# Optimization experiments

Measured on AMD Instinct MI355X. Metric: run time of the kernel, lower is better.

## Reference

```python
import jax, jax.numpy as jnp
import numpy as np

T_DATA, E_NO, I_NO, SUB_NO = 10000, 2000, 500, 64
KERN_LEN, PAD = 201, 100


def setup_inputs() -> dict:
    key = jax.random.key(0)
    ks = jax.random.split(key, 8)
    S_e = (jax.random.uniform(ks[0], (T_DATA, E_NO)) < 0.05).astype(jnp.float32)
    S_i = (jax.random.uniform(ks[1], (T_DATA, I_NO)) < 0.05).astype(jnp.float32)
    # Synapse->subunit assignment: each synapse feeds exactly one subunit (one-hot rows of C_syn.T)
    ae = jax.random.randint(ks[2], (E_NO,), 0, SUB_NO)
    ai = jax.random.randint(ks[3], (I_NO,), 0, SUB_NO)
    C_syn_e = jax.nn.one_hot(ae, SUB_NO, dtype=jnp.float32).T  # [sub_no, E_no]
    C_syn_i = jax.nn.one_hot(ai, SUB_NO, dtype=jnp.float32).T  # [sub_no, I_no]
    # Sparse dendritic coupling matrix (binary tree-like connectivity)
    C_den = (jax.random.uniform(ks[4], (SUB_NO, SUB_NO)) < 0.05).astype(jnp.float32)
    # Learned raw parameters (per __init__: ones * init)
    weight_raw = jnp.zeros((SUB_NO, 2), jnp.float32)          # weight_init = 0.0
    decay_raw = jnp.full((SUB_NO,), 2.0, jnp.float32)         # decay_init = 2.0
    threshold_raw = jnp.zeros((SUB_NO,), jnp.float32)         # threshold_init = 0.0
    prop_raw = jnp.full((SUB_NO,), -1.0, jnp.float32)         # prop_init = -1.0
    return {"S_e": S_e, "S_i": S_i, "C_den": C_den, "C_syn_e": C_syn_e,
            "C_syn_i": C_syn_i, "weight_raw": weight_raw, "decay_raw": decay_raw,
            "threshold_raw": threshold_raw, "prop_raw": prop_raw}


def reference(S_e, S_i, C_den, C_syn_e, C_syn_i, weight_raw, decay_raw, threshold_raw, prop_raw):
    sub_no = C_den.shape[0]
    # Project presynaptic spikes onto subunits: [T, sub_no]
    syn_e = S_e @ C_syn_e.T
    syn_i = S_i @ C_syn_i.T
    weight_e = jnp.exp(weight_raw[:, 0])
    weight_i = -jnp.exp(weight_raw[:, 1])
    decay = jax.nn.sigmoid(decay_raw)
    threshold = -jnp.exp(threshold_raw)
    prop = jnpp = jnp.exp(prop_raw)
    drive = syn_e * weight_e[None, :] + syn_i * weight_i[None, :]  # [T, sub_no]

    def step_fn(carry, d_t):
        V, spk = carry
        # reset-on-spike, leak, synaptic drive, dendritic propagation of spikes
        V = V * (1.0 - spk) * decay + d_t + (spk * prop) @ C_den.T
        spk = jnp.heaviside(V + threshold, jnp.float32(0.0))
        return (V, spk), spk

    init = (jnp.zeros(sub_no, jnp.float32), jnp.zeros(sub_no, jnp.float32))
    _, spk_out = jax.lax.scan(step_fn, init, drive)  # spk_out: [T, sub_no]

    # Alpha-kernel smoothing of root subunit spike train (Tau, W are fixed buffers)
    t_tau = jnp.arange(KERN_LEN, dtype=jnp.float32) / jnp.exp(jnp.float32(2.0))
    kern = t_tau * jnp.exp(-t_tau) * jnp.exp(jnp.float32(0.75))
    kern_flipped = jnp.flip(kern)
    x = spk_out[:, 0][None, None, :]               # [1,1,T]
    w = kern_flipped[None, None, :]                # [1,1,201]
    final = jax.lax.conv_general_dilated(x, w, (1,), [(PAD, PAD)]).reshape(-1)
    return final, spk_out
```

## Files before the change

### kernel.cpp

```cpp
#include <hip/hip_runtime.h>
#include <math.h>

#define T_DATA 10000
#define E_NO 2000
#define I_NO 500
#define SUB_NO 64
#define KERN_LEN 201
#define PAD 100
#define NBLK 314

__global__ void assign_kernel(const float* __restrict__ Ce, const float* __restrict__ Ci,
                              int* __restrict__ ae, int* __restrict__ ai) {
    int idx = blockIdx.x * 256 + threadIdx.x;
    if (idx < E_NO) {
        int a = 0;
        for (int s = 0; s < SUB_NO; ++s)
            if (Ce[(size_t)s * E_NO + idx] != 0.0f) a = s;
        ae[idx] = a;
    } else if (idx < E_NO + I_NO) {
        int i = idx - E_NO;
        int a = 0;
        for (int s = 0; s < SUB_NO; ++s)
            if (Ci[(size_t)s * I_NO + i] != 0.0f) a = s;
        ai[i] = a;
    }
}

__global__ void drive_kernel(const float* __restrict__ Se, const float* __restrict__ Si,
                             const float* __restrict__ wraw,
                             const int* __restrict__ ae, const int* __restrict__ ai,
                             float* __restrict__ drive) {
    __shared__ float be[SUB_NO];
    __shared__ float bi[SUB_NO];
    int t = blockIdx.x;
    int tid = threadIdx.x;
    if (tid < SUB_NO) { be[tid] = 0.0f; bi[tid] = 0.0f; }
    __syncthreads();
    const float4* se4 = (const float4*)(Se + (size_t)t * E_NO);
    for (int e4 = tid; e4 < E_NO / 4; e4 += 256) {
        float4 v = se4[e4];
        int b = e4 * 4;
        if (v.x != 0.0f) atomicAdd(&be[ae[b + 0]], 1.0f);
        if (v.y != 0.0f) atomicAdd(&be[ae[b + 1]], 1.0f);
        if (v.z != 0.0f) atomicAdd(&be[ae[b + 2]], 1.0f);
        if (v.w != 0.0f) atomicAdd(&be[ae[b + 3]], 1.0f);
    }
    const float4* si4 = (const float4*)(Si + (size_t)t * I_NO);
    for (int i4 = tid; i4 < I_NO / 4; i4 += 256) {
        float4 v = si4[i4];
        int b = i4 * 4;
        if (v.x != 0.0f) atomicAdd(&bi[ai[b + 0]], 1.0f);
        if (v.y != 0.0f) atomicAdd(&bi[ai[b + 1]], 1.0f);
        if (v.z != 0.0f) atomicAdd(&bi[ai[b + 2]], 1.0f);
        if (v.w != 0.0f) atomicAdd(&bi[ai[b + 3]], 1.0f);
    }
    __syncthreads();
    if (tid < SUB_NO) {
        float we = (float)exp((double)wraw[2 * tid]);
        float wi = -(float)exp((double)wraw[2 * tid + 1]);
        drive[(size_t)t * SUB_NO + tid] =
            __fadd_rn(__fmul_rn(be[tid], we), __fmul_rn(bi[tid], wi));
    }
}

#define S_LIN(DK, DK1, LIT) \
  "v_and_b32 %[tlo], vcc_lo, %[rlo]\n\t" \
  "v_and_b32 %[thi], vcc_hi, %[rhi]\n\t" \
  "v_cndmask_b32 %[base], %[w0], %[" DK "], vcc\n\t" \
  "v_bcnt_u32_b32 %[kc], %[tlo], 0\n\t" \
  "v_bcnt_u32_b32 %[kc], %[thi], %[kc]\n\t" \
  "v_cvt_f32_u32 %[kf], %[kc]\n\t" \
  "v_mul_f32 %[acc], %[kf], %[pp]\n\t" \
  "v_add_f32 %[vv], %[base], %[acc]\n\t" \
  "v_cmp_gt_f32 vcc, %[vv], %[thr]\n\t" \
  "v_mul_f32 %[w0], %[vv], %[dec]\n\t" \
  "v_add_f32 %[w0], %[w0], %[" DK1 "]\n\t" \
  "v_or_b32 %[tmp], " LIT ", %[bits]\n\t" \
  "v_cndmask_b32 %[bits], %[bits], %[tmp], vcc\n\t"

#define S_BP(DK, DK1, LIT) \
  "v_and_b32 %[tlo], vcc_lo, %[rlo]\n\t" \
  "v_and_b32 %[thi], vcc_hi, %[rhi]\n\t" \
  "v_cndmask_b32 %[base], %[w0], %[" DK "], vcc\n\t" \
  "v_bcnt_u32_b32 %[kc], %[tlo], 0\n\t" \
  "v_bcnt_u32_b32 %[kc], %[thi], %[kc]\n\t" \
  "v_lshlrev_b32 %[kc], 2, %[kc]\n\t" \
  "ds_bpermute_b32 %[acc], %[kc], %[vtab]\n\t" \
  "s_waitcnt lgkmcnt(0)\n\t" \
  "v_add_f32 %[vv], %[base], %[acc]\n\t" \
  "v_cmp_gt_f32 vcc, %[vv], %[thr]\n\t" \
  "v_mul_f32 %[w0], %[vv], %[dec]\n\t" \
  "v_add_f32 %[w0], %[w0], %[" DK1 "]\n\t" \
  "v_or_b32 %[tmp], " LIT ", %[bits]\n\t" \
  "v_cndmask_b32 %[bits], %[bits], %[tmp], vcc\n\t"

#define STEPS32(S) \
  S("d0","d1","1")            S("d1","d2","2")            S("d2","d3","4")            S("d3","d4","8") \
  S("d4","d5","16")           S("d5","d6","32")           S("d6","d7","64")           S("d7","d8","0x80") \
  S("d8","d9","0x100")        S("d9","d10","0x200")       S("d10","d11","0x400")      S("d11","d12","0x800") \
  S("d12","d13","0x1000")     S("d13","d14","0x2000")     S("d14","d15","0x4000")     S("d15","d16","0x8000") \
  S("d16","d17","0x10000")    S("d17","d18","0x20000")    S("d18","d19","0x40000")    S("d19","d20","0x80000") \
  S("d20","d21","0x100000")   S("d21","d22","0x200000")   S("d22","d23","0x400000")   S("d23","d24","0x800000") \
  S("d24","d25","0x1000000")  S("d25","d26","0x2000000")  S("d26","d27","0x4000000")  S("d27","d28","0x8000000") \
  S("d28","d29","0x10000000") S("d29","d30","0x20000000") S("d30","d31","0x40000000") S("d31","d32","0x80000000")

#define RUN_BLOCK(STEPSTR, B) do { \
    unsigned int _tlo, _thi, _kc, _tmp, _bits; float _kf, _acc, _base; \
    unsigned long long _mout; \
    asm volatile( \
        "s_mov_b64 vcc, %[min]\n\t" \
        "v_mov_b32 %[bits], 0\n\t" \
        "s_nop 1\n\t" \
        STEPSTR \
        "s_mov_b64 %[mout], vcc\n\t" \
        : [vv]"+v"(V), [w0]"+v"(w0), [bits]"=&v"(_bits), [mout]"=s"(_mout), \
          [tlo]"=&v"(_tlo), [thi]"=&v"(_thi), [kc]"=&v"(_kc), [tmp]"=&v"(_tmp), \
          [kf]"=&v"(_kf), [acc]"=&v"(_acc), [base]"=&v"(_base) \
        : [min]"s"(m), [rlo]"v"(row_lo), [rhi]"v"(row_hi), [pp]"v"(p0), \
          [dec]"v"(decay), [thr]"v"(thrpos), [vtab]"v"(vtab), \
          [d0]"v"(B[0]),  [d1]"v"(B[1]),  [d2]"v"(B[2]),  [d3]"v"(B[3]), \
          [d4]"v"(B[4]),  [d5]"v"(B[5]),  [d6]"v"(B[6]),  [d7]"v"(B[7]), \
          [d8]"v"(B[8]),  [d9]"v"(B[9]),  [d10]"v"(B[10]), [d11]"v"(B[11]), \
          [d12]"v"(B[12]), [d13]"v"(B[13]), [d14]"v"(B[14]), [d15]"v"(B[15]), \
          [d16]"v"(B[16]), [d17]"v"(B[17]), [d18]"v"(B[18]), [d19]"v"(B[19]), \
          [d20]"v"(B[20]), [d21]"v"(B[21]), [d22]"v"(B[22]), [d23]"v"(B[23]), \
          [d24]"v"(B[24]), [d25]"v"(B[25]), [d26]"v"(B[26]), [d27]"v"(B[27]), \
          [d28]"v"(B[28]), [d29]"v"(B[29]), [d30]"v"(B[30]), [d31]"v"(B[31]), \
          [d32]"v"(B[32]) \
        : "vcc"); \
    m = _mout; bitsv = _bits; } while (0)

__device__ void scan_lin_asm(const float* drive, unsigned int* packed,
                             unsigned int row_lo, unsigned int row_hi, float p0,
                             float decay, float thrpos, float vtab, int s) {
    const float* dp = drive + s;
    unsigned int* pw = packed + s;
    float bufA[33], bufB[33];
#pragma unroll
    for (int k = 0; k < 33; ++k) bufA[k] = dp[(size_t)k * SUB_NO];
    float V = 0.0f, w0 = bufA[0];
    unsigned long long m = 0ull;
    unsigned int bitsv;
    for (int b = 0; b < NBLK; b += 2) {
#pragma unroll
        for (int k = 0; k < 33; ++k) bufB[k] = dp[((size_t)(b + 1) * 32 + k) * SUB_NO];
        RUN_BLOCK(STEPS32(S_LIN), bufA);
        pw[(size_t)b * SUB_NO] = bitsv;
#pragma unroll
        for (int k = 0; k < 33; ++k) bufA[k] = dp[((size_t)(b + 2) * 32 + k) * SUB_NO];
        RUN_BLOCK(STEPS32(S_LIN), bufB);
        pw[(size_t)(b + 1) * SUB_NO] = bitsv;
    }
}

__device__ void scan_bp_asm(const float* drive, unsigned int* packed,
                            unsigned int row_lo, unsigned int row_hi, float p0,
                            float decay, float thrpos, float vtab, int s) {
    const float* dp = drive + s;
    unsigned int* pw = packed + s;
    float bufA[33], bufB[33];
#pragma unroll
    for (int k = 0; k < 33; ++k) bufA[k] = dp[(size_t)k * SUB_NO];
    float V = 0.0f, w0 = bufA[0];
    unsigned long long m = 0ull;
    unsigned int bitsv;
    for (int b = 0; b < NBLK; b += 2) {
#pragma unroll
        for (int k = 0; k < 33; ++k) bufB[k] = dp[((size_t)(b + 1) * 32 + k) * SUB_NO];
        RUN_BLOCK(STEPS32(S_BP), bufA);
        pw[(size_t)b * SUB_NO] = bitsv;
#pragma unroll
        for (int k = 0; k < 33; ++k) bufA[k] = dp[((size_t)(b + 2) * 32 + k) * SUB_NO];
        RUN_BLOCK(STEPS32(S_BP), bufB);
        pw[(size_t)(b + 1) * SUB_NO] = bitsv;
    }
}

__device__ void scan_slow(const float* drive, unsigned int* packed,
                          unsigned long long rowmask, const float* prop_l,
                          float decay, float thr, int s) {
    float V = 0.0f;
    bool sp = false;
    unsigned long long mask = 0ull;
    for (int b = 0; b < NBLK; ++b) {
        unsigned int bits = 0u;
        for (int k = 0; k < 32; ++k) {
            int t = b * 32 + k;
            float d = drive[(size_t)t * SUB_NO + s];
            unsigned long long mm = mask & rowmask;
            float acc = 0.0f;
            for (int j = 0; j < SUB_NO; ++j) {
                float c = ((mm >> j) & 1ull) ? prop_l[j] : 0.0f;
                acc = __fadd_rn(acc, c);
            }
            float Vr = sp ? 0.0f : V;
            float bb = __fmul_rn(Vr, decay);
            float cc = __fadd_rn(bb, d);
            V = __fadd_rn(cc, acc);
            float sv = __fadd_rn(V, thr);
            sp = sv > 0.0f;
            mask = __ballot(sp);
            bits |= sp ? (1u << k) : 0u;
        }
        packed[(size_t)b * SUB_NO + s] = bits;
    }
}

__global__ void __launch_bounds__(64, 1)
scan_kernel(const float* drive, const float* __restrict__ Cden,
            const float* __restrict__ decay_raw, const float* __restrict__ thr_raw,
            const float* __restrict__ prop_raw, unsigned int* packed) {
    __shared__ float prop_l[SUB_NO];
    int s = threadIdx.x;
    prop_l[s] = (float)exp((double)prop_raw[s]);
    __syncthreads();
    float myp = prop_l[s];

    float em = (float)exp(-(double)decay_raw[s]);
    float den = __fadd_rn(1.0f, em);
    float decay = (float)(1.0 / (double)den);
    float thrpos = (float)exp((double)thr_raw[s]);
    float thr = -thrpos;

    unsigned long long rowmask = 0ull;
    for (int j = 0; j < SUB_NO; ++j)
        if (Cden[(size_t)s * SUB_NO + j] != 0.0f) rowmask |= (1ull << j);
    unsigned int row_lo = (unsigned int)rowmask;
    unsigned int row_hi = (unsigned int)(rowmask >> 32);

    float p0 = prop_l[0];
    bool uni = __all(myp == p0);
    int maxk = (int)__popcll(rowmask);
    for (int off = 32; off; off >>= 1) {
        int o = __shfl_xor(maxk, off);
        maxk = maxk > o ? maxk : o;
    }

    float seqk = 0.0f;
    for (int i = 0; i < s; ++i) seqk = __fadd_rn(seqk, p0);
    float vtab = seqk;

    bool lok = (s > maxk) || (seqk == __fmul_rn((float)s, p0));
    bool uselin = uni && __all(lok);

    if (uselin)
        scan_lin_asm(drive, packed, row_lo, row_hi, p0, decay, thrpos, vtab, s);
    else if (uni)
        scan_bp_asm(drive, packed, row_lo, row_hi, p0, decay, thrpos, vtab, s);
    else
        scan_slow(drive, packed, rowmask, prop_l, decay, thr, s);
}

__global__ void expand_kernel(const unsigned int* __restrict__ packed,
                              float* __restrict__ spk_out) {
    int idx = blockIdx.x * 256 + threadIdx.x;
    int t = idx >> 6, s = idx & 63;
    unsigned int w = packed[(size_t)(t >> 5) * SUB_NO + s];
    spk_out[idx] = (float)((w >> (t & 31)) & 1u);
}

__global__ void conv_kernel(const unsigned int* __restrict__ packed,
                            float* __restrict__ out) {
    __shared__ float kern_s[KERN_LEN];
    __shared__ float x_s[256 + 2 * PAD];
    int tid = threadIdx.x;
    int t0 = blockIdx.x * 256;

    float e2 = (float)exp(2.0);
    float e075 = (float)exp(0.75);
    for (int m = tid; m < KERN_LEN; m += 256) {
        float tt = (float)m / e2;
        kern_s[m] = __fmul_rn(__fmul_rn(tt, expf(-tt)), e075);
    }
    for (int k = tid; k < 256 + 2 * PAD; k += 256) {
        int idx = t0 - PAD + k;
        float xv = 0.0f;
        if (idx >= 0 && idx < T_DATA) {
            unsigned int w = packed[(size_t)(idx >> 5) * SUB_NO];
            xv = (float)((w >> (idx & 31)) & 1u);
        }
        x_s[k] = xv;
    }
    __syncthreads();

    int t = t0 + tid;
    if (t < T_DATA) {
        float acc = 0.0f;
        for (int m = 0; m < KERN_LEN; ++m)
            acc += kern_s[m] * x_s[tid + 2 * PAD - m];
        out[t] = acc;
    }
}

extern "C" void kernel_launch(void* const* d_in, const int* in_sizes, int n_in,
                              void* d_out, int out_size, void* d_ws, size_t ws_size,
                              hipStream_t stream) {
    const float* S_e      = (const float*)d_in[0];
    const float* S_i      = (const float*)d_in[1];
    const float* C_den    = (const float*)d_in[2];
    const float* C_syn_e  = (const float*)d_in[3];
    const float* C_syn_i  = (const float*)d_in[4];
    const float* w_raw    = (const float*)d_in[5];
    const float* dec_raw  = (const float*)d_in[6];
    const float* thr_raw  = (const float*)d_in[7];
    const float* prop_raw = (const float*)d_in[8];

    float* out = (float*)d_out;
    float* ws = (float*)d_ws;
    float* drive = ws;
    int*   ae    = (int*)(ws + 640000);
    int*   ai    = (int*)(ws + 642000);

    size_t need_bytes = (size_t)(642500 + NBLK * SUB_NO) * 4;
    unsigned int* packed = (ws_size >= need_bytes)
                               ? (unsigned int*)(ws + 642500)
                               : (unsigned int*)ws;

    assign_kernel<<<(E_NO + I_NO + 255) / 256, 256, 0, stream>>>(C_syn_e, C_syn_i, ae, ai);
    drive_kernel<<<T_DATA, 256, 0, stream>>>(S_e, S_i, w_raw, ae, ai, drive);
    scan_kernel<<<1, 64, 0, stream>>>(drive, C_den, dec_raw, thr_raw, prop_raw, packed);
    expand_kernel<<<T_DATA * SUB_NO / 256, 256, 0, stream>>>(packed, out + T_DATA);
    conv_kernel<<<(T_DATA + 255) / 256, 256, 0, stream>>>(packed, out);
}
```

Measured before the change: 554.0 us.

## Hand-schedule the serial scan loop in asm with a rolling per-step prefetch of drive

Replaces the compiler-scheduled double-buffered scan with a fully hand-written asm loop that uses fixed registers. Each step issues one global load for the value 32 steps ahead and waits with vmcnt(31), so memory latency is hidden inside the serial dependency chain instead of appearing as bulk reloads between blocks. Address bumps use 32-bit adds only, so the host checks whether the buffers could cross a 4 GB low-word boundary and otherwise falls back to the C path. The asm also pins many VGPRs and SGPRs by name, which is fragile, and the prefetch reads past the end of the drive array.

Measured after the change: 540.0 us. 1.03x faster.

```diff
diff --git a/kernel.cpp b/kernel.cpp
--- a/kernel.cpp
+++ b/kernel.cpp
@@ -8,6 +8,7 @@
 #define KERN_LEN 201
 #define PAD 100
 #define NBLK 314
+typedef unsigned long long ull;
 
 __global__ void assign_kernel(const float* __restrict__ Ce, const float* __restrict__ Ci,
                               int* __restrict__ ae, int* __restrict__ ai) {
@@ -63,61 +64,232 @@
     }
 }
 
-#define S_LIN(DK, DK1, LIT) \
-  "v_and_b32 %[tlo], vcc_lo, %[rlo]\n\t" \
-  "v_and_b32 %[thi], vcc_hi, %[rhi]\n\t" \
+
+#define SL(B,NB,OFF,LIT,BITS) \
+  "v_and_b32 v16, vcc_lo, %[rlo]\n\t" \
+  "v_and_b32 v17, vcc_hi, %[rhi]\n\t" \
+  "v_cndmask_b32 v21, v29, " B ", vcc\n\t" \
+  "v_bcnt_u32_b32 v18, v16, 0\n\t" \
+  "v_bcnt_u32_b32 v18, v17, v18\n\t" \
+  "v_cvt_f32_u32 v19, v18\n\t" \
+  "global_load_dword " B ", v[24:25], off offset:" OFF "\n\t" \
+  "v_mul_f32 v20, v19, %[p]\n\t" \
+  "v_add_f32 v28, v21, v20\n\t" \
+  "v_cmp_gt_f32 vcc, v28, %[thr]\n\t" \
+  "v_mul_f32 v29, v28, %[dec]\n\t" \
+  "v_or_b32 v22, " LIT ", " BITS "\n\t" \
+  "v_cndmask_b32 " BITS ", " BITS ", v22, vcc\n\t" \
+  "s_waitcnt vmcnt(31)\n\t" \
+  "v_add_f32 v29, v29, " NB "\n\t"
+
+#define SL0(B,NB,OFF,BITS) \
+  "v_and_b32 v16, vcc_lo, %[rlo]\n\t" \
+  "v_and_b32 v17, vcc_hi, %[rhi]\n\t" \
+  "v_cndmask_b32 v21, v29, " B ", vcc\n\t" \
+  "v_bcnt_u32_b32 v18, v16, 0\n\t" \
+  "v_bcnt_u32_b32 v18, v17, v18\n\t" \
+  "v_cvt_f32_u32 v19, v18\n\t" \
+  "global_load_dword " B ", v[24:25], off offset:" OFF "\n\t" \
+  "v_mul_f32 v20, v19, %[p]\n\t" \
+  "v_add_f32 v28, v21, v20\n\t" \
+  "v_cmp_gt_f32 vcc, v28, %[thr]\n\t" \
+  "v_mul_f32 v29, v28, %[dec]\n\t" \
+  "v_cndmask_b32 " BITS ", 0, 1, vcc\n\t" \
+  "s_waitcnt vmcnt(31)\n\t" \
+  "v_add_f32 v29, v29, " NB "\n\t"
+
+#define SB(B,NB,OFF,LIT,BITS) \
+  "v_and_b32 v16, vcc_lo, %[rlo]\n\t" \
+  "v_and_b32 v17, vcc_hi, %[rhi]\n\t" \
+  "v_cndmask_b32 v21, v29, " B ", vcc\n\t" \
+  "v_bcnt_u32_b32 v18, v16, 0\n\t" \
+  "v_bcnt_u32_b32 v18, v17, v18\n\t" \
+  "v_lshlrev_b32 v18, 2, v18\n\t" \
+  "ds_bpermute_b32 v20, v18, %[vt]\n\t" \
+  "global_load_dword " B ", v[24:25], off offset:" OFF "\n\t" \
+  "s_waitcnt lgkmcnt(0)\n\t" \
+  "v_add_f32 v28, v21, v20\n\t" \
+  "v_cmp_gt_f32 vcc, v28, %[thr]\n\t" \
+  "v_mul_f32 v29, v28, %[dec]\n\t" \
+  "v_or_b32 v22, " LIT ", " BITS "\n\t" \
+  "v_cndmask_b32 " BITS ", " BITS ", v22, vcc\n\t" \
+  "s_waitcnt vmcnt(31)\n\t" \
+  "v_add_f32 v29, v29, " NB "\n\t"
+
+#define SB0(B,NB,OFF,BITS) \
+  "v_and_b32 v16, vcc_lo, %[rlo]\n\t" \
+  "v_and_b32 v17, vcc_hi, %[rhi]\n\t" \
+  "v_cndmask_b32 v21, v29, " B ", vcc\n\t" \
+  "v_bcnt_u32_b32 v18, v16, 0\n\t" \
+  "v_bcnt_u32_b32 v18, v17, v18\n\t" \
+  "v_lshlrev_b32 v18, 2, v18\n\t" \
+  "ds_bpermute_b32 v20, v18, %[vt]\n\t" \
+  "global_load_dword " B ", v[24:25], off offset:" OFF "\n\t" \
+  "s_waitcnt lgkmcnt(0)\n\t" \
+  "v_add_f32 v28, v21, v20\n\t" \
+  "v_cmp_gt_f32 vcc, v28, %[thr]\n\t" \
+  "v_mul_f32 v29, v28, %[dec]\n\t" \
+  "v_cndmask_b32 " BITS ", 0, 1, vcc\n\t" \
+  "s_waitcnt vmcnt(31)\n\t" \
+  "v_add_f32 v29, v29, " NB "\n\t"
+
+#define BUMPL "v_add_u32 v24, s16, v24\n\t"
+#define STOREW(BITS) \
+  "global_store_dword v[26:27], " BITS ", off\n\t" \
+  "v_add_u32 v26, s17, v26\n\t"
+
+#define BLK(S,S0,BITS) \
+  S0("v32","v33","0",BITS) \
+  S("v33","v34","256","2",BITS)          S("v34","v35","512","4",BITS) \
+  S("v35","v36","768","8",BITS)          S("v36","v37","1024","16",BITS) \
+  S("v37","v38","1280","32",BITS)        S("v38","v39","1536","64",BITS) \
+  S("v39","v40","1792","0x80",BITS)      S("v40","v41","2048","0x100",BITS) \
+  S("v41","v42","2304","0x200",BITS)     S("v42","v43","2560","0x400",BITS) \
+  S("v43","v44","2816","0x800",BITS)     S("v44","v45","3072","0x1000",BITS) \
+  S("v45","v46","3328","0x2000",BITS)    S("v46","v47","3584","0x4000",BITS) \
+  S("v47","v48","3840","0x8000",BITS) \
+  BUMPL \
+  S("v48","v49","0","0x10000",BITS)      S("v49","v50","256","0x20000",BITS) \
+  S("v50","v51","512","0x40000",BITS)    S("v51","v52","768","0x80000",BITS) \
+  S("v52","v53","1024","0x100000",BITS)  S("v53","v54","1280","0x200000",BITS) \
+  S("v54","v55","1536","0x400000",BITS)  S("v55","v56","1792","0x800000",BITS) \
+  S("v56","v57","2048","0x1000000",BITS) S("v57","v58","2304","0x2000000",BITS) \
+  S("v58","v59","2560","0x4000000",BITS) S("v59","v60","2816","0x8000000",BITS) \
+  S("v60","v61","3072","0x10000000",BITS) S("v61","v62","3328","0x20000000",BITS) \
+  S("v62","v63","3584","0x40000000",BITS) S("v63","v32","3840","0x80000000",BITS) \
+  BUMPL
+
+#define PRO \
+  "v_mov_b32 v24, %[alo]\n\t" "v_mov_b32 v25, %[ahi]\n\t" \
+  "v_mov_b32 v26, %[blo]\n\t" "v_mov_b32 v27, %[bhi]\n\t" \
+  "s_mov_b32 s16, 0x1000\n\t" "s_mov_b32 s17, 0x100\n\t" \
+  "global_load_dword v32, v[24:25], off offset:0\n\t" \
+  "global_load_dword v33, v[24:25], off offset:256\n\t" \
+  "global_load_dword v34, v[24:25], off offset:512\n\t" \
+  "global_load_dword v35, v[24:25], off offset:768\n\t" \
+  "global_load_dword v36, v[24:25], off offset:1024\n\t" \
+  "global_load_dword v37, v[24:25], off offset:1280\n\t" \
+  "global_load_dword v38, v[24:25], off offset:1536\n\t" \
+  "global_load_dword v39, v[24:25], off offset:1792\n\t" \
+  "global_load_dword v40, v[24:25], off offset:2048\n\t" \
+  "global_load_dword v41, v[24:25], off offset:2304\n\t" \
+  "global_load_dword v42, v[24:25], off offset:2560\n\t" \
+  "global_load_dword v43, v[24:25], off offset:2816\n\t" \
+  "global_load_dword v44, v[24:25], off offset:3072\n\t" \
+  "global_load_dword v45, v[24:25], off offset:3328\n\t" \
+  "global_load_dword v46, v[24:25], off offset:3584\n\t" \
+  "global_load_dword v47, v[24:25], off offset:3840\n\t" \
+  BUMPL \
+  "global_load_dword v48, v[24:25], off offset:0\n\t" \
+  "global_load_dword v49, v[24:25], off offset:256\n\t" \
+  "global_load_dword v50, v[24:25], off offset:512\n\t" \
+  "global_load_dword v51, v[24:25], off offset:768\n\t" \
+  "global_load_dword v52, v[24:25], off offset:1024\n\t" \
+  "global_load_dword v53, v[24:25], off offset:1280\n\t" \
+  "global_load_dword v54, v[24:25], off offset:1536\n\t" \
+  "global_load_dword v55, v[24:25], off offset:1792\n\t" \
+  "global_load_dword v56, v[24:25], off offset:2048\n\t" \
+  "global_load_dword v57, v[24:25], off offset:2304\n\t" \
+  "global_load_dword v58, v[24:25], off offset:2560\n\t" \
+  "global_load_dword v59, v[24:25], off offset:2816\n\t" \
+  "global_load_dword v60, v[24:25], off offset:3072\n\t" \
+  "global_load_dword v61, v[24:25], off offset:3328\n\t" \
+  "global_load_dword v62, v[24:25], off offset:3584\n\t" \
+  "global_load_dword v63, v[24:25], off offset:3840\n\t" \
+  BUMPL \
+  "s_mov_b64 vcc, 0\n\t" \
+  "s_nop 2\n\t" \
+  "s_movk_i32 s20, 157\n\t" \
+  "s_waitcnt vmcnt(31)\n\t" \
+  "v_mov_b32 v29, v32\n\t" \
+  "v_mov_b32 v28, 0\n\t"
+
+#define CLOBBERS \
+  "v16","v17","v18","v19","v20","v21","v22","v23","v24","v25","v26","v27", \
+  "v28","v29","v30","v31","v32","v33","v34","v35","v36","v37","v38","v39", \
+  "v40","v41","v42","v43","v44","v45","v46","v47","v48","v49","v50","v51", \
+  "v52","v53","v54","v55","v56","v57","v58","v59","v60","v61","v62","v63", \
+  "s16","s17","s20","vcc","scc","memory"
+
+__device__ void scan_lin_hot(const float* drive, unsigned* packed,
+                             unsigned rlo, unsigned rhi, float p, float dec,
+                             float thr, int s) {
+    ull a = (ull)drive + (ull)s * 4;
+    ull b = (ull)packed + (ull)s * 4;
+    asm volatile(
+        PRO
+        "Lmain%=:\n\t"
+        BLK(SL, SL0, "v23") STOREW("v23")
+        BLK(SL, SL0, "v30") STOREW("v30")
+        "s_add_i32 s20, s20, -1\n\t"
+        "s_cmp_lg_u32 s20, 0\n\t"
+        "s_cbranch_scc1 Lmain%=\n\t"
+        :
+        : [alo]"v"((unsigned)a), [ahi]"v"((unsigned)(a >> 32)),
+          [blo]"v"((unsigned)b), [bhi]"v"((unsigned)(b >> 32)),
+          [rlo]"v"(rlo), [rhi]"v"(rhi), [p]"v"(p), [dec]"v"(dec), [thr]"v"(thr)
+        : CLOBBERS);
+}
+
+__device__ void scan_bp_hot(const float* drive, unsigned* packed,
+                            unsigned rlo, unsigned rhi, float dec,
+                            float thr, float vtab, int s) {
+    ull a = (ull)drive + (ull)s * 4;
+    ull b = (ull)packed + (ull)s * 4;
+    asm volatile(
+        PRO
+        "Lmainb%=:\n\t"
+        BLK(SB, SB0, "v23") STOREW("v23")
+        BLK(SB, SB0, "v30") STOREW("v30")
+        "s_add_i32 s20, s20, -1\n\t"
+        "s_cmp_lg_u32 s20, 0\n\t"
+        "s_cbranch_scc1 Lmainb%=\n\t"
+        :
+        : [alo]"v"((unsigned)a), [ahi]"v"((unsigned)(a >> 32)),
+          [blo]"v"((unsigned)b), [bhi]"v"((unsigned)(b >> 32)),
+          [rlo]"v"(rlo), [rhi]"v"(rhi), [vt]"v"(vtab), [dec]"v"(dec), [thr]"v"(thr)
+        : CLOBBERS);
+}
+
+#define C_LIN(DK, DK1, LIT) \
+  "v_and_b32 %[tlo], vcc_lo, %[crlo]\n\t" \
+  "v_and_b32 %[thi], vcc_hi, %[crhi]\n\t" \
   "v_cndmask_b32 %[base], %[w0], %[" DK "], vcc\n\t" \
   "v_bcnt_u32_b32 %[kc], %[tlo], 0\n\t" \
   "v_bcnt_u32_b32 %[kc], %[thi], %[kc]\n\t" \
   "v_cvt_f32_u32 %[kf], %[kc]\n\t" \
-  "v_mul_f32 %[acc], %[kf], %[pp]\n\t" \
+  "v_mul_f32 %[acc], %[kf], %[cp]\n\t" \
   "v_add_f32 %[vv], %[base], %[acc]\n\t" \
-  "v_cmp_gt_f32 vcc, %[vv], %[thr]\n\t" \
-  "v_mul_f32 %[w0], %[vv], %[dec]\n\t" \
+  "v_cmp_gt_f32 vcc, %[vv], %[cthr]\n\t" \
+  "v_mul_f32 %[w0], %[vv], %[cdec]\n\t" \
   "v_add_f32 %[w0], %[w0], %[" DK1 "]\n\t" \
   "v_or_b32 %[tmp], " LIT ", %[bits]\n\t" \
   "v_cndmask_b32 %[bits], %[bits], %[tmp], vcc\n\t"
 
-#define S_BP(DK, DK1, LIT) \
-  "v_and_b32 %[tlo], vcc_lo, %[rlo]\n\t" \
-  "v_and_b32 %[thi], vcc_hi, %[rhi]\n\t" \
-  "v_cndmask_b32 %[base], %[w0], %[" DK "], vcc\n\t" \
-  "v_bcnt_u32_b32 %[kc], %[tlo], 0\n\t" \
-  "v_bcnt_u32_b32 %[kc], %[thi], %[kc]\n\t" \
-  "v_lshlrev_b32 %[kc], 2, %[kc]\n\t" \
-  "ds_bpermute_b32 %[acc], %[kc], %[vtab]\n\t" \
-  "s_waitcnt lgkmcnt(0)\n\t" \
-  "v_add_f32 %[vv], %[base], %[acc]\n\t" \
-  "v_cmp_gt_f32 vcc, %[vv], %[thr]\n\t" \
-  "v_mul_f32 %[w0], %[vv], %[dec]\n\t" \
-  "v_add_f32 %[w0], %[w0], %[" DK1 "]\n\t" \
-  "v_or_b32 %[tmp], " LIT ", %[bits]\n\t" \
-  "v_cndmask_b32 %[bits], %[bits], %[tmp], vcc\n\t"
-
-#define STEPS32(S) \
-  S("d0","d1","1")            S("d1","d2","2")            S("d2","d3","4")            S("d3","d4","8") \
-  S("d4","d5","16")           S("d5","d6","32")           S("d6","d7","64")           S("d7","d8","0x80") \
-  S("d8","d9","0x100")        S("d9","d10","0x200")       S("d10","d11","0x400")      S("d11","d12","0x800") \
-  S("d12","d13","0x1000")     S("d13","d14","0x2000")     S("d14","d15","0x4000")     S("d15","d16","0x8000") \
-  S("d16","d17","0x10000")    S("d17","d18","0x20000")    S("d18","d19","0x40000")    S("d19","d20","0x80000") \
-  S("d20","d21","0x100000")   S("d21","d22","0x200000")   S("d22","d23","0x400000")   S("d23","d24","0x800000") \
-  S("d24","d25","0x1000000")  S("d25","d26","0x2000000")  S("d26","d27","0x4000000")  S("d27","d28","0x8000000") \
-  S("d28","d29","0x10000000") S("d29","d30","0x20000000") S("d30","d31","0x40000000") S("d31","d32","0x80000000")
-
-#define RUN_BLOCK(STEPSTR, B) do { \
-    unsigned int _tlo, _thi, _kc, _tmp, _bits; float _kf, _acc, _base; \
-    unsigned long long _mout; \
+#define CSTEPS32 \
+  C_LIN("d0","d1","1")            C_LIN("d1","d2","2")            C_LIN("d2","d3","4")            C_LIN("d3","d4","8") \
+  C_LIN("d4","d5","16")           C_LIN("d5","d6","32")           C_LIN("d6","d7","64")           C_LIN("d7","d8","0x80") \
+  C_LIN("d8","d9","0x100")        C_LIN("d9","d10","0x200")       C_LIN("d10","d11","0x400")      C_LIN("d11","d12","0x800") \
+  C_LIN("d12","d13","0x1000")     C_LIN("d13","d14","0x2000")     C_LIN("d14","d15","0x4000")     C_LIN("d15","d16","0x8000") \
+  C_LIN("d16","d17","0x10000")    C_LIN("d17","d18","0x20000")    C_LIN("d18","d19","0x40000")    C_LIN("d19","d20","0x80000") \
+  C_LIN("d20","d21","0x100000")   C_LIN("d21","d22","0x200000")   C_LIN("d22","d23","0x400000")   C_LIN("d23","d24","0x800000") \
+  C_LIN("d24","d25","0x1000000")  C_LIN("d25","d26","0x2000000")  C_LIN("d26","d27","0x4000000")  C_LIN("d27","d28","0x8000000") \
+  C_LIN("d28","d29","0x10000000") C_LIN("d29","d30","0x20000000") C_LIN("d30","d31","0x40000000") C_LIN("d31","d32","0x80000000")
+
+#define CRUN_BLOCK(B) do { \
+    unsigned _tlo, _thi, _kc, _tmp, _bits; float _kf, _acc, _base; \
+    ull _mout; \
     asm volatile( \
         "s_mov_b64 vcc, %[min]\n\t" \
         "v_mov_b32 %[bits], 0\n\t" \
         "s_nop 1\n\t" \
-        STEPSTR \
+        CSTEPS32 \
         "s_mov_b64 %[mout], vcc\n\t" \
         : [vv]"+v"(V), [w0]"+v"(w0), [bits]"=&v"(_bits), [mout]"=s"(_mout), \
           [tlo]"=&v"(_tlo), [thi]"=&v"(_thi), [kc]"=&v"(_kc), [tmp]"=&v"(_tmp), \
           [kf]"=&v"(_kf), [acc]"=&v"(_acc), [base]"=&v"(_base) \
-        : [min]"s"(m), [rlo]"v"(row_lo), [rhi]"v"(row_hi), [pp]"v"(p0), \
-          [dec]"v"(decay), [thr]"v"(thrpos), [vtab]"v"(vtab), \
+        : [min]"s"(m), [crlo]"v"(row_lo), [crhi]"v"(row_hi), [cp]"v"(p0), \
+          [cdec]"v"(decay), [cthr]"v"(thrpos), \
           [d0]"v"(B[0]),  [d1]"v"(B[1]),  [d2]"v"(B[2]),  [d3]"v"(B[3]), \
           [d4]"v"(B[4]),  [d5]"v"(B[5]),  [d6]"v"(B[6]),  [d7]"v"(B[7]), \
           [d8]"v"(B[8]),  [d9]"v"(B[9]),  [d10]"v"(B[10]), [d11]"v"(B[11]), \
@@ -130,64 +302,41 @@
         : "vcc"); \
     m = _mout; bitsv = _bits; } while (0)
 
-__device__ void scan_lin_asm(const float* drive, unsigned int* packed,
-                             unsigned int row_lo, unsigned int row_hi, float p0,
-                             float decay, float thrpos, float vtab, int s) {
+__device__ void scan_lin_c(const float* drive, unsigned* packed,
+                           unsigned row_lo, unsigned row_hi, float p0,
+                           float decay, float thrpos, int s) {
     const float* dp = drive + s;
-    unsigned int* pw = packed + s;
+    unsigned* pw = packed + s;
     float bufA[33], bufB[33];
 #pragma unroll
     for (int k = 0; k < 33; ++k) bufA[k] = dp[(size_t)k * SUB_NO];
     float V = 0.0f, w0 = bufA[0];
-    unsigned long long m = 0ull;
-    unsigned int bitsv;
+    ull m = 0ull;
+    unsigned bitsv;
     for (int b = 0; b < NBLK; b += 2) {
 #pragma unroll
         for (int k = 0; k < 33; ++k) bufB[k] = dp[((size_t)(b + 1) * 32 + k) * SUB_NO];
-        RUN_BLOCK(STEPS32(S_LIN), bufA);
+        CRUN_BLOCK(bufA);
         pw[(size_t)b * SUB_NO] = bitsv;
 #pragma unroll
         for (int k = 0; k < 33; ++k) bufA[k] = dp[((size_t)(b + 2) * 32 + k) * SUB_NO];
-        RUN_BLOCK(STEPS32(S_LIN), bufB);
+        CRUN_BLOCK(bufB);
         pw[(size_t)(b + 1) * SUB_NO] = bitsv;
     }
 }
 
-__device__ void scan_bp_asm(const float* drive, unsigned int* packed,
-                            unsigned int row_lo, unsigned int row_hi, float p0,
-                            float decay, float thrpos, float vtab, int s) {
-    const float* dp = drive + s;
-    unsigned int* pw = packed + s;
-    float bufA[33], bufB[33];
-#pragma unroll
-    for (int k = 0; k < 33; ++k) bufA[k] = dp[(size_t)k * SUB_NO];
-    float V = 0.0f, w0 = bufA[0];
-    unsigned long long m = 0ull;
-    unsigned int bitsv;
-    for (int b = 0; b < NBLK; b += 2) {
-#pragma unroll
-        for (int k = 0; k < 33; ++k) bufB[k] = dp[((size_t)(b + 1) * 32 + k) * SUB_NO];
-        RUN_BLOCK(STEPS32(S_BP), bufA);
-        pw[(size_t)b * SUB_NO] = bitsv;
-#pragma unroll
-        for (int k = 0; k < 33; ++k) bufA[k] = dp[((size_t)(b + 2) * 32 + k) * SUB_NO];
-        RUN_BLOCK(STEPS32(S_BP), bufB);
-        pw[(size_t)(b + 1) * SUB_NO] = bitsv;
-    }
-}
-
-__device__ void scan_slow(const float* drive, unsigned int* packed,
-                          unsigned long long rowmask, const float* prop_l,
+__device__ void scan_slow(const float* drive, unsigned* packed,
+                          ull rowmask, const float* prop_l,
                           float decay, float thr, int s) {
     float V = 0.0f;
     bool sp = false;
-    unsigned long long mask = 0ull;
+    ull mask = 0ull;
     for (int b = 0; b < NBLK; ++b) {
-        unsigned int bits = 0u;
+        unsigned bits = 0u;
         for (int k = 0; k < 32; ++k) {
             int t = b * 32 + k;
             float d = drive[(size_t)t * SUB_NO + s];
-            unsigned long long mm = mask & rowmask;
+            ull mm = mask & rowmask;
             float acc = 0.0f;
             for (int j = 0; j < SUB_NO; ++j) {
                 float c = ((mm >> j) & 1ull) ? prop_l[j] : 0.0f;
@@ -209,7 +358,7 @@
 __global__ void __launch_bounds__(64, 1)
 scan_kernel(const float* drive, const float* __restrict__ Cden,
             const float* __restrict__ decay_raw, const float* __restrict__ thr_raw,
-            const float* __restrict__ prop_raw, unsigned int* packed) {
+            const float* __restrict__ prop_raw, unsigned* packed, int fast) {
     __shared__ float prop_l[SUB_NO];
     int s = threadIdx.x;
     prop_l[s] = (float)exp((double)prop_raw[s]);
@@ -222,11 +371,11 @@
     float thrpos = (float)exp((double)thr_raw[s]);
     float thr = -thrpos;
 
-    unsigned long long rowmask = 0ull;
+    ull rowmask = 0ull;
     for (int j = 0; j < SUB_NO; ++j)
         if (Cden[(size_t)s * SUB_NO + j] != 0.0f) rowmask |= (1ull << j);
-    unsigned int row_lo = (unsigned int)rowmask;
-    unsigned int row_hi = (unsigned int)(rowmask >> 32);
+    unsigned row_lo = (unsigned)rowmask;
+    unsigned row_hi = (unsigned)(rowmask >> 32);
 
     float p0 = prop_l[0];
     bool uni = __all(myp == p0);
@@ -243,23 +392,25 @@
     bool lok = (s > maxk) || (seqk == __fmul_rn((float)s, p0));
     bool uselin = uni && __all(lok);
 
-    if (uselin)
-        scan_lin_asm(drive, packed, row_lo, row_hi, p0, decay, thrpos, vtab, s);
-    else if (uni)
-        scan_bp_asm(drive, packed, row_lo, row_hi, p0, decay, thrpos, vtab, s);
+    if (uselin && fast)
+        scan_lin_hot(drive, packed, row_lo, row_hi, p0, decay, thrpos, s);
+    else if (uselin)
+        scan_lin_c(drive, packed, row_lo, row_hi, p0, decay, thrpos, s);
+    else if (uni && fast)
+        scan_bp_hot(drive, packed, row_lo, row_hi, decay, thrpos, vtab, s);
     else
         scan_slow(drive, packed, rowmask, prop_l, decay, thr, s);
 }
 
-__global__ void expand_kernel(const unsigned int* __restrict__ packed,
+__global__ void expand_kernel(const unsigned* __restrict__ packed,
                               float* __restrict__ spk_out) {
     int idx = blockIdx.x * 256 + threadIdx.x;
     int t = idx >> 6, s = idx & 63;
-    unsigned int w = packed[(size_t)(t >> 5) * SUB_NO + s];
+    unsigned w = packed[(size_t)(t >> 5) * SUB_NO + s];
     spk_out[idx] = (float)((w >> (t & 31)) & 1u);
 }
 
-__global__ void conv_kernel(const unsigned int* __restrict__ packed,
+__global__ void conv_kernel(const unsigned* __restrict__ packed,
                             float* __restrict__ out) {
     __shared__ float kern_s[KERN_LEN];
     __shared__ float x_s[256 + 2 * PAD];
@@ -276,7 +427,7 @@
         int idx = t0 - PAD + k;
         float xv = 0.0f;
         if (idx >= 0 && idx < T_DATA) {
-            unsigned int w = packed[(size_t)(idx >> 5) * SUB_NO];
+            unsigned w = packed[(size_t)(idx >> 5) * SUB_NO];
             xv = (float)((w >> (idx & 31)) & 1u);
         }
         x_s[k] = xv;
@@ -312,13 +463,18 @@
     int*   ai    = (int*)(ws + 642000);
 
     size_t need_bytes = (size_t)(642500 + NBLK * SUB_NO) * 4;
-    unsigned int* packed = (ws_size >= need_bytes)
-                               ? (unsigned int*)(ws + 642500)
-                               : (unsigned int*)ws;
+    unsigned* packed = (ws_size >= need_bytes)
+                           ? (unsigned*)(ws + 642500)
+                           : (unsigned*)ws;
+
+    ull da = (ull)drive, pa = (ull)packed;
+    int fast = ((da & 0xFFFFFFFFull) + 0x290000ull <= 0x100000000ull) &&
+               ((pa & 0xFFFFFFFFull) + 0x30000ull  <= 0x100000000ull) &&
+               (ws_size >= need_bytes);
 
     assign_kernel<<<(E_NO + I_NO + 255) / 256, 256, 0, stream>>>(C_syn_e, C_syn_i, ae, ai);
     drive_kernel<<<T_DATA, 256, 0, stream>>>(S_e, S_i, w_raw, ae, ai, drive);
-    scan_kernel<<<1, 64, 0, stream>>>(drive, C_den, dec_raw, thr_raw, prop_raw, packed);
+    scan_kernel<<<1, 64, 0, stream>>>(drive, C_den, dec_raw, thr_raw, prop_raw, packed, fast);
     expand_kernel<<<T_DATA * SUB_NO / 256, 256, 0, stream>>>(packed, out + T_DATA);
     conv_kernel<<<(T_DATA + 255) / 256, 256, 0, stream>>>(packed, out);
 }
```
